# Kernel tuning notes

Hardware: AMD Instinct MI355X
Metric: run time of the kernel (lower is better)

The kernel has to match this reference:

```python
import jax, jax.numpy as jnp
import numpy as np

B, T, I, H, O = 64, 512, 128, 1024, 128
FORGET_BIAS = 1.0  # TF LSTMCell default


def setup_inputs() -> dict:
    key = jax.random.key(0)
    k1, k2, k3 = jax.random.split(key, 3)
    X = jax.random.normal(k1, (B, T, I), dtype=jnp.float32)
    Wk = jax.random.normal(k2, (I + H, 4 * H), dtype=jnp.float32) * 0.02
    b = jnp.zeros((4 * H,), dtype=jnp.float32)
    Wd = jax.random.normal(k3, (H, O), dtype=jnp.float32) * 0.02
    bd = jnp.zeros((O,), dtype=jnp.float32)
    return {"X": X, "Wk": Wk, "b": b, "Wd": Wd, "bd": bd}


def _lstm(X, Wk, b):
    # TF LSTMCell with activation=relu; gate order in kernel: i, j, f, o
    batch = X.shape[0]
    h = X.shape[-1]  # not used; keep shapes explicit below
    c0 = jnp.zeros((batch, H), dtype=X.dtype)
    h0 = jnp.zeros((batch, H), dtype=X.dtype)

    def step(carry, x_t):
        c, hs = carry
        z = jnp.concatenate([x_t, hs], axis=-1) @ Wk + b  # [B, 4H]
        i, j, f, o = jnp.split(z, 4, axis=-1)
        i = jax.nn.sigmoid(i)
        f = jax.nn.sigmoid(f + FORGET_BIAS)
        o = jax.nn.sigmoid(o)
        g = jax.nn.relu(j)          # cell-input activation (custom relu)
        c_new = f * c + i * g
        h_new = o * jax.nn.relu(c_new)  # output activation (custom relu)
        return (c_new, h_new), h_new

    xs = jnp.swapaxes(X, 0, 1)  # [T, B, I]
    _, hs = jax.lax.scan(step, (c0, h0), xs)
    return jnp.swapaxes(hs, 0, 1)  # [B, T, H]


def reference(X, Wk, b, Wd, bd):
    rnn_out = _lstm(X, Wk, b)          # [B, T, H]
    outputs = rnn_out @ Wd + bd        # [B, T, O] (SL=True: dense per timestep)
    return outputs
```

## Files before the change

### kernel.cpp

```cpp
#include <hip/hip_runtime.h>
#include <math.h>

#define Bsz 64
#define Tn  512
#define In  128
#define Hn  1024
#define KT  1152
#define NBLK 128

#define GARR0 0

typedef __attribute__((ext_vector_type(8))) short bf16x8;
typedef __attribute__((ext_vector_type(4))) short s16x4;
typedef __attribute__((ext_vector_type(4))) float f32x4;
typedef __attribute__((ext_vector_type(4))) int   i32x4;

__device__ void llvm_amdgcn_raw_buffer_store_i16(short vdata, i32x4 srsrc, int voffset, int soffset, int cpol) __asm("llvm.amdgcn.raw.buffer.store.i16");

__device__ __forceinline__ i32x4 make_srd(const void* p, int bytes) {
  i32x4 r;
  r.x = (int)(unsigned)(unsigned long long)p;
  r.y = (int)((unsigned long long)p >> 32);
  r.z = bytes;
  r.w = 0x00020000;
  return r;
}

__device__ __forceinline__ unsigned short f2bf(float f) {
  union { float f; unsigned u; } x; x.f = f;
  unsigned r = x.u + 0x7FFFu + ((x.u >> 16) & 1u);
  return (unsigned short)(r >> 16);
}
__device__ __forceinline__ float sigmoidf_(float x) { return 1.0f / (1.0f + __expf(-x)); }

__global__ __launch_bounds__(256) void cast_x_kernel(const float* __restrict__ in,
                                                     unsigned short* __restrict__ out) {
  int i = blockIdx.x * 256 + threadIdx.x;
  f32x4 v = ((const f32x4*)in)[i];
  s16x4 o;
  o.x = (short)f2bf(v.x); o.y = (short)f2bf(v.y);
  o.z = (short)f2bf(v.z); o.w = (short)f2bf(v.w);
  ((s16x4*)out)[i] = o;
}

__global__ __launch_bounds__(256) void transpose_cast_kernel(const float* __restrict__ in,
                                                             unsigned short* __restrict__ out,
                                                             int R, int C, int ldo, int tilesR) {
  __shared__ unsigned short tile[64][73];
  int br = blockIdx.x % tilesR, bc = blockIdx.x / tilesR;
  int r0 = br << 6, c0 = bc << 6;
  for (int e = threadIdx.x; e < 4096; e += 256) {
    int r = e >> 6, c = e & 63;
    tile[r][c] = f2bf(in[(size_t)(r0 + r) * C + (c0 + c)]);
  }
  __syncthreads();
  for (int e = threadIdx.x; e < 4096; e += 256) {
    int c = e >> 6, r = e & 63;
    out[(size_t)(c0 + c) * ldo + (r0 + r)] = tile[r][c];
  }
}

__global__ __launch_bounds__(512, 1) void lstm_kernel(
    const unsigned short* __restrict__ Xb,
    const unsigned short* __restrict__ WkT,
    const float* __restrict__ bias,
    unsigned short* __restrict__ hs,
    unsigned* __restrict__ S)
{
  __shared__ float Z4[4][64][36];
  const int tid = threadIdx.x;
  const int blk = blockIdx.x;
  const int grp = blk >> 4;
  const int w   = tid >> 6;
  const int mh  = w & 1;
  const int kq  = w >> 1;
  const int l   = tid & 63, q = l >> 4, n16 = l & 15;

  const i32x4 hsrd = make_srd(hs, Tn * Bsz * Hn * 2);

  bf16x8 Bf[2][9];
#pragma unroll
  for (int nt = 0; nt < 2; ++nt) {
    int cl   = nt * 16 + n16;
    int gcol = (cl >> 3) * Hn + blk * 8 + (cl & 7);
    const unsigned short* bp = WkT + (size_t)gcol * KT;
    Bf[nt][0] = *(const bf16x8*)(bp + kq * 32 + q * 8);
#pragma unroll
    for (int ks = 1; ks < 9; ++ks)
      Bf[nt][ks] = *(const bf16x8*)(bp + 128 + kq * 256 + (ks - 1) * 32 + q * 8);
  }

  const int eb = tid >> 3, ej = tid & 7;
  const float bi  = bias[           blk * 8 + ej];
  const float bg  = bias[    Hn   + blk * 8 + ej];
  const float bfg = bias[2 * Hn   + blk * 8 + ej] + 1.0f;
  const float bo  = bias[3 * Hn   + blk * 8 + ej];
  const int   hst_off = (eb * Hn + blk * 8 + ej) * 2;
  float cst = 0.0f;

  const int b0 = mh * 32 + n16;
  const int b1 = b0 + 16;

  for (int t = 0; t < Tn; ++t) {
    f32x4 a00 = {0,0,0,0}, a01 = {0,0,0,0}, a10 = {0,0,0,0}, a11 = {0,0,0,0};

    bf16x8 X0 = *(const bf16x8*)(Xb + ((size_t)b0 * Tn + t) * In + kq * 32 + q * 8);
    bf16x8 X1 = *(const bf16x8*)(Xb + ((size_t)b1 * Tn + t) * In + kq * 32 + q * 8);

    if (t > 0) {
      const unsigned tgt = 16u * (unsigned)t;
      for (;;) {
        unsigned f = (l < 2) ? __hip_atomic_load(&S[GARR0 + 32 * (2 * kq + l)],
                                                 __ATOMIC_RELAXED, __HIP_MEMORY_SCOPE_AGENT)
                             : 0xFFFFFFFFu;
        if (__ballot(f >= tgt) == ~0ull) break;
        __builtin_amdgcn_s_sleep(1);
      }
      const unsigned short* hrow = hs + (size_t)(t - 1) * (Bsz * Hn);
      a00 = __builtin_amdgcn_mfma_f32_16x16x32_bf16(X0, Bf[0][0], a00, 0, 0, 0);
      a01 = __builtin_amdgcn_mfma_f32_16x16x32_bf16(X0, Bf[1][0], a01, 0, 0, 0);
      a10 = __builtin_amdgcn_mfma_f32_16x16x32_bf16(X1, Bf[0][0], a10, 0, 0, 0);
      a11 = __builtin_amdgcn_mfma_f32_16x16x32_bf16(X1, Bf[1][0], a11, 0, 0, 0);
#pragma unroll
      for (int ks = 1; ks < 9; ++ks) {
        int kh = kq * 256 + (ks - 1) * 32 + q * 8;
        bf16x8 A0 = *(const bf16x8*)(hrow + (size_t)b0 * Hn + kh);
        bf16x8 A1 = *(const bf16x8*)(hrow + (size_t)b1 * Hn + kh);
        a00 = __builtin_amdgcn_mfma_f32_16x16x32_bf16(A0, Bf[0][ks], a00, 0, 0, 0);
        a01 = __builtin_amdgcn_mfma_f32_16x16x32_bf16(A0, Bf[1][ks], a01, 0, 0, 0);
        a10 = __builtin_amdgcn_mfma_f32_16x16x32_bf16(A1, Bf[0][ks], a10, 0, 0, 0);
        a11 = __builtin_amdgcn_mfma_f32_16x16x32_bf16(A1, Bf[1][ks], a11, 0, 0, 0);
      }
    } else {
      a00 = __builtin_amdgcn_mfma_f32_16x16x32_bf16(X0, Bf[0][0], a00, 0, 0, 0);
      a01 = __builtin_amdgcn_mfma_f32_16x16x32_bf16(X0, Bf[1][0], a01, 0, 0, 0);
      a10 = __builtin_amdgcn_mfma_f32_16x16x32_bf16(X1, Bf[0][0], a10, 0, 0, 0);
      a11 = __builtin_amdgcn_mfma_f32_16x16x32_bf16(X1, Bf[1][0], a11, 0, 0, 0);
    }

#pragma unroll
    for (int r = 0; r < 4; ++r) {
      int row = mh * 32 + q * 4 + r;
      Z4[kq][row     ][     n16] = a00[r];
      Z4[kq][row     ][16 + n16] = a01[r];
      Z4[kq][row + 16][     n16] = a10[r];
      Z4[kq][row + 16][16 + n16] = a11[r];
    }
    __syncthreads();

    float zi = bi, zg = bg, zf = bfg, zo = bo;
#pragma unroll
    for (int k2 = 0; k2 < 4; ++k2) {
      zi += Z4[k2][eb][     ej];
      zg += Z4[k2][eb][ 8 + ej];
      zf += Z4[k2][eb][16 + ej];
      zo += Z4[k2][eb][24 + ej];
    }
    float ig = sigmoidf_(zi);
    float g  = fmaxf(zg, 0.0f);
    float ff = sigmoidf_(zf);
    float oo = sigmoidf_(zo);
    cst = ff * cst + ig * g;
    float hn = oo * fmaxf(cst, 0.0f);
    llvm_amdgcn_raw_buffer_store_i16((short)f2bf(hn), hsrd,
                                     t * (Bsz * Hn * 2) + hst_off, 0, 17);

    __syncthreads();
    if (t < Tn - 1 && tid == 0) {
      (void)__hip_atomic_fetch_add(&S[GARR0 + 32 * grp], 1u,
                                   __ATOMIC_RELAXED, __HIP_MEMORY_SCOPE_AGENT);
    }
  }
}

__global__ __launch_bounds__(256) void dense_kernel(
    const unsigned short* __restrict__ hs,
    const unsigned short* __restrict__ WdT,
    const float* __restrict__ bd,
    float* __restrict__ out)
{
  const int tid = threadIdx.x;
  const int w = tid >> 6, l = tid & 63, q = l >> 4, n16 = l & 15;
  const int R0 = blockIdx.x * 64 + w * 16;
  f32x4 acc[8];
#pragma unroll
  for (int i = 0; i < 8; ++i) acc[i] = (f32x4){0, 0, 0, 0};
  const unsigned short* arow = hs + (size_t)(R0 + n16) * Hn + q * 8;
#pragma unroll 4
  for (int ks = 0; ks < 32; ++ks) {
    bf16x8 A = *(const bf16x8*)(arow + ks * 32);
#pragma unroll
    for (int nt = 0; nt < 8; ++nt) {
      bf16x8 Bf = *(const bf16x8*)(WdT + (size_t)(nt * 16 + n16) * Hn + ks * 32 + q * 8);
      acc[nt] = __builtin_amdgcn_mfma_f32_16x16x32_bf16(A, Bf, acc[nt], 0, 0, 0);
    }
  }
#pragma unroll
  for (int nt = 0; nt < 8; ++nt) {
    int col = nt * 16 + n16;
    float bdv = bd[col];
#pragma unroll
    for (int r = 0; r < 4; ++r) {
      int R = R0 + q * 4 + r;
      int b = R & 63, t = R >> 6;
      out[((size_t)b * Tn + t) * 128 + col] = acc[nt][r] + bdv;
    }
  }
}

extern "C" void kernel_launch(void* const* d_in, const int* in_sizes, int n_in,
                              void* d_out, int out_size, void* d_ws, size_t ws_size,
                              hipStream_t stream) {
  const float* X    = (const float*)d_in[0];
  const float* Wk   = (const float*)d_in[1];
  const float* bias = (const float*)d_in[2];
  const float* Wd   = (const float*)d_in[3];
  const float* bd   = (const float*)d_in[4];
  float* out = (float*)d_out;

  char* ws = (char*)d_ws;
  unsigned short* Xb  = (unsigned short*)(ws);
  unsigned short* WkT = (unsigned short*)(ws + 8388608);
  unsigned short* WdT = (unsigned short*)(ws + 17825792);
  unsigned short* hs  = (unsigned short*)(ws + 18087936);
  unsigned*       syn = (unsigned*)      (ws + 85196800);

  hipMemsetAsync(syn, 0, 4096, stream);
  cast_x_kernel<<<4096, 256, 0, stream>>>(X, Xb);
  transpose_cast_kernel<<<1152, 256, 0, stream>>>(Wk, WkT, 1152, 4096, 1152, 18);
  transpose_cast_kernel<<<32, 256, 0, stream>>>(Wd, WdT, 1024, 128, 1024, 16);
  lstm_kernel<<<NBLK, 512, 0, stream>>>(Xb, WkT, bias, hs, syn);
  dense_kernel<<<512, 256, 0, stream>>>(hs, WdT, bd, out);
}
```

Measured before the change: 3.602 ms.

## Replace atomic counter sync with sentinel-filled hidden state polling

Drops the per-group atomic counters between LSTM blocks. The hidden-state buffer is prefilled with 0xFF (a negative-NaN bf16 sentinel), and each wave spins by reloading its slice of h with cache-bypassing buffer loads until no sign-bit sentinel remains, then feeds those loaded values straight into the MFMAs. The input-projection MFMAs are hoisted ahead of the wait, and the __syncthreads calls become raw s_barrier with an lgkmcnt wait. This adds a 64 MB memset each launch and relies on real h values never having the sign bit set, which holds since h = sigmoid times relu is non-negative, and on the 16-byte loads seeing complete writes.

```diff
diff --git a/kernel.cpp b/kernel.cpp
--- a/kernel.cpp
+++ b/kernel.cpp
@@ -8,14 +8,13 @@
 #define KT  1152
 #define NBLK 128
 
-#define GARR0 0
-
 typedef __attribute__((ext_vector_type(8))) short bf16x8;
 typedef __attribute__((ext_vector_type(4))) short s16x4;
 typedef __attribute__((ext_vector_type(4))) float f32x4;
 typedef __attribute__((ext_vector_type(4))) int   i32x4;
 
 __device__ void llvm_amdgcn_raw_buffer_store_i16(short vdata, i32x4 srsrc, int voffset, int soffset, int cpol) __asm("llvm.amdgcn.raw.buffer.store.i16");
+__device__ i32x4 llvm_amdgcn_raw_buffer_load_v4i32(i32x4 srsrc, int voffset, int soffset, int cpol) __asm("llvm.amdgcn.raw.buffer.load.v4i32");
 
 __device__ __forceinline__ i32x4 make_srd(const void* p, int bytes) {
   i32x4 r;
@@ -24,6 +23,10 @@
   r.z = bytes;
   r.w = 0x00020000;
   return r;
+}
+
+__device__ __forceinline__ bf16x8 as_bf16x8(i32x4 v) {
+  union { i32x4 i; bf16x8 b; } u; u.i = v; return u.b;
 }
 
 __device__ __forceinline__ unsigned short f2bf(float f) {
@@ -70,7 +73,6 @@
   __shared__ float Z4[4][64][36];
   const int tid = threadIdx.x;
   const int blk = blockIdx.x;
-  const int grp = blk >> 4;
   const int w   = tid >> 6;
   const int mh  = w & 1;
   const int kq  = w >> 1;
@@ -100,42 +102,47 @@
 
   const int b0 = mh * 32 + n16;
   const int b1 = b0 + 16;
+  const int ho0 = (b0 * Hn + kq * 256 + q * 8) * 2;
+  const int ho1 = (b1 * Hn + kq * 256 + q * 8) * 2;
 
   for (int t = 0; t < Tn; ++t) {
     f32x4 a00 = {0,0,0,0}, a01 = {0,0,0,0}, a10 = {0,0,0,0}, a11 = {0,0,0,0};
 
     bf16x8 X0 = *(const bf16x8*)(Xb + ((size_t)b0 * Tn + t) * In + kq * 32 + q * 8);
     bf16x8 X1 = *(const bf16x8*)(Xb + ((size_t)b1 * Tn + t) * In + kq * 32 + q * 8);
+    a00 = __builtin_amdgcn_mfma_f32_16x16x32_bf16(X0, Bf[0][0], a00, 0, 0, 0);
+    a01 = __builtin_amdgcn_mfma_f32_16x16x32_bf16(X0, Bf[1][0], a01, 0, 0, 0);
+    a10 = __builtin_amdgcn_mfma_f32_16x16x32_bf16(X1, Bf[0][0], a10, 0, 0, 0);
+    a11 = __builtin_amdgcn_mfma_f32_16x16x32_bf16(X1, Bf[1][0], a11, 0, 0, 0);
 
     if (t > 0) {
-      const unsigned tgt = 16u * (unsigned)t;
+      const int tb = (t - 1) * (Bsz * Hn * 2);
+      i32x4 H0[8], H1[8];
       for (;;) {
-        unsigned f = (l < 2) ? __hip_atomic_load(&S[GARR0 + 32 * (2 * kq + l)],
-                                                 __ATOMIC_RELAXED, __HIP_MEMORY_SCOPE_AGENT)
-                             : 0xFFFFFFFFu;
-        if (__ballot(f >= tgt) == ~0ull) break;
+        asm volatile("" ::: "memory");
+#pragma unroll
+        for (int ks = 0; ks < 8; ++ks) {
+          H0[ks] = llvm_amdgcn_raw_buffer_load_v4i32(hsrd, tb + ho0 + ks * 64, 0, 17);
+          H1[ks] = llvm_amdgcn_raw_buffer_load_v4i32(hsrd, tb + ho1 + ks * 64, 0, 17);
+        }
+        int bad = 0;
+#pragma unroll
+        for (int ks = 0; ks < 8; ++ks) {
+          bad |= H0[ks].x | H0[ks].y | H0[ks].z | H0[ks].w;
+          bad |= H1[ks].x | H1[ks].y | H1[ks].z | H1[ks].w;
+        }
+        if (__ballot(((unsigned)bad & 0x80008000u) == 0u) == ~0ull) break;
         __builtin_amdgcn_s_sleep(1);
       }
-      const unsigned short* hrow = hs + (size_t)(t - 1) * (Bsz * Hn);
-      a00 = __builtin_amdgcn_mfma_f32_16x16x32_bf16(X0, Bf[0][0], a00, 0, 0, 0);
-      a01 = __builtin_amdgcn_mfma_f32_16x16x32_bf16(X0, Bf[1][0], a01, 0, 0, 0);
-      a10 = __builtin_amdgcn_mfma_f32_16x16x32_bf16(X1, Bf[0][0], a10, 0, 0, 0);
-      a11 = __builtin_amdgcn_mfma_f32_16x16x32_bf16(X1, Bf[1][0], a11, 0, 0, 0);
-#pragma unroll
-      for (int ks = 1; ks < 9; ++ks) {
-        int kh = kq * 256 + (ks - 1) * 32 + q * 8;
-        bf16x8 A0 = *(const bf16x8*)(hrow + (size_t)b0 * Hn + kh);
-        bf16x8 A1 = *(const bf16x8*)(hrow + (size_t)b1 * Hn + kh);
-        a00 = __builtin_amdgcn_mfma_f32_16x16x32_bf16(A0, Bf[0][ks], a00, 0, 0, 0);
-        a01 = __builtin_amdgcn_mfma_f32_16x16x32_bf16(A0, Bf[1][ks], a01, 0, 0, 0);
-        a10 = __builtin_amdgcn_mfma_f32_16x16x32_bf16(A1, Bf[0][ks], a10, 0, 0, 0);
-        a11 = __builtin_amdgcn_mfma_f32_16x16x32_bf16(A1, Bf[1][ks], a11, 0, 0, 0);
+#pragma unroll
+      for (int ks = 0; ks < 8; ++ks) {
+        bf16x8 A0 = as_bf16x8(H0[ks]);
+        bf16x8 A1 = as_bf16x8(H1[ks]);
+        a00 = __builtin_amdgcn_mfma_f32_16x16x32_bf16(A0, Bf[0][ks + 1], a00, 0, 0, 0);
+        a01 = __builtin_amdgcn_mfma_f32_16x16x32_bf16(A0, Bf[1][ks + 1], a01, 0, 0, 0);
+        a10 = __builtin_amdgcn_mfma_f32_16x16x32_bf16(A1, Bf[0][ks + 1], a10, 0, 0, 0);
+        a11 = __builtin_amdgcn_mfma_f32_16x16x32_bf16(A1, Bf[1][ks + 1], a11, 0, 0, 0);
       }
-    } else {
-      a00 = __builtin_amdgcn_mfma_f32_16x16x32_bf16(X0, Bf[0][0], a00, 0, 0, 0);
-      a01 = __builtin_amdgcn_mfma_f32_16x16x32_bf16(X0, Bf[1][0], a01, 0, 0, 0);
-      a10 = __builtin_amdgcn_mfma_f32_16x16x32_bf16(X1, Bf[0][0], a10, 0, 0, 0);
-      a11 = __builtin_amdgcn_mfma_f32_16x16x32_bf16(X1, Bf[1][0], a11, 0, 0, 0);
     }
 
 #pragma unroll
@@ -146,7 +153,8 @@
       Z4[kq][row + 16][     n16] = a10[r];
       Z4[kq][row + 16][16 + n16] = a11[r];
     }
-    __syncthreads();
+    asm volatile("s_waitcnt lgkmcnt(0)" ::: "memory");
+    __builtin_amdgcn_s_barrier();
 
     float zi = bi, zg = bg, zf = bfg, zo = bo;
 #pragma unroll
@@ -165,11 +173,8 @@
     llvm_amdgcn_raw_buffer_store_i16((short)f2bf(hn), hsrd,
                                      t * (Bsz * Hn * 2) + hst_off, 0, 17);
 
-    __syncthreads();
-    if (t < Tn - 1 && tid == 0) {
-      (void)__hip_atomic_fetch_add(&S[GARR0 + 32 * grp], 1u,
-                                   __ATOMIC_RELAXED, __HIP_MEMORY_SCOPE_AGENT);
-    }
+    asm volatile("s_waitcnt lgkmcnt(0)" ::: "memory");
+    __builtin_amdgcn_s_barrier();
   }
 }
 
@@ -225,6 +230,7 @@
   unsigned short* hs  = (unsigned short*)(ws + 18087936);
   unsigned*       syn = (unsigned*)      (ws + 85196800);
 
+  hipMemsetAsync(hs, 0xFF, 67108864, stream);
   hipMemsetAsync(syn, 0, 4096, stream);
   cast_x_kernel<<<4096, 256, 0, stream>>>(X, Xb);
   transpose_cast_kernel<<<1152, 256, 0, stream>>>(Wk, WkT, 1152, 4096, 1152, 18);
```

Measured after the change: 3.068 ms. -14.8%, faster.
